# Performance work log

Hardware: AMD Instinct MI355X
Metric: run time of the kernel (lower is better)

## Reference

```python
import jax, jax.numpy as jnp
import numpy as np

IN_DIM = 256
CODE_LEN = 128
MEM_LEN = 65536
BETA = 1.0


def setup_inputs() -> dict:
    key = jax.random.key(0)
    k1, k2, k3, k4, k5, k6 = jax.random.split(key, 6)
    x = jax.random.normal(k1, (1, IN_DIM), dtype=jnp.float32)
    memory = jax.random.normal(k2, (MEM_LEN, CODE_LEN), dtype=jnp.float32)
    mem_data = jax.random.normal(k3, (MEM_LEN, IN_DIM), dtype=jnp.float32)
    mem_idx = jnp.arange(MEM_LEN, dtype=jnp.int64) if jax.config.jax_enable_x64 else jnp.arange(MEM_LEN, dtype=jnp.int32)
    W = jax.random.normal(k4, (CODE_LEN, IN_DIM), dtype=jnp.float32) / np.sqrt(IN_DIM)
    b = jax.random.normal(k5, (CODE_LEN,), dtype=jnp.float32) * 0.01
    count = jnp.array(0, dtype=jnp.int32)
    return {"x": x, "memory": memory, "mem_data": mem_data, "mem_idx": mem_idx,
            "W": W, "b": b, "count": count}


def reference(x, memory, mem_data, mem_idx, W, b, count):
    # mean/std normalization using memory bank statistics (torch .std uses ddof=1)
    mean = mem_data.mean(axis=0)                      # [in_dim]
    std = mem_data.std(axis=0, ddof=1)                # [in_dim]
    new = (x - mean) / std
    new = jnp.where(std == 0, 0.0, new)               # [1, in_dim]
    # linear encode
    enc = new @ W.T + b                               # [1, code_len]
    # L1 distance to every memory slot, take min
    dists = jnp.sum(jnp.abs(memory - enc), axis=1)    # [mem_len]
    loss = dists.min()
    # conditional scatter update of memory / mem_data / mem_idx
    do_update = loss <= BETA
    pos = jnp.argmin(mem_idx)
    new_memory = jnp.where(do_update,
                           memory.at[pos].set(enc[0]), memory)
    new_mem_data = jnp.where(do_update,
                             mem_data.at[pos].set(x[0]), mem_data)
    new_mem_idx = jnp.where(do_update,
                            mem_idx.at[pos].set(count.astype(mem_idx.dtype)), mem_idx)
    return loss, new_memory, new_mem_data, new_mem_idx
```

## Files before the change

kernel.cpp:

```cpp
#include <hip/hip_runtime.h>
#include <hip/hip_bf16.h>

#define IN_DIM   256
#define CODE_LEN 128
#define MEM_LEN  65536
#define BETA     1.0f

#define OUT_MEM_OFF   1
#define OUT_MD_OFF    (1 + MEM_LEN*CODE_LEN)
#define OUT_IDX_OFF   (OUT_MD_OFF + MEM_LEN*IN_DIM)

#define WS_COLSUM 0
#define WS_COLSQ  256
#define WS_ENC    512
#define WS_LOSS   640
#define WS_KEY    642

#define MD_ELEMS  (MEM_LEN*IN_DIM)
#define MD_TILES  ((MD_ELEMS-4)/4)
#define MEM_ELEMS (MEM_LEN*CODE_LEN)
#define MEM_STORE_TILES 2097151

__device__ __forceinline__ float4 load4u(const float* p) {
    float4 v; v.x = p[0]; v.y = p[1]; v.z = p[2]; v.w = p[3]; return v;
}

__global__ __launch_bounds__(512, 4) void k_stats_copy(
        const float* __restrict__ mem_data,
        const int*   __restrict__ mem_idx,
        float* __restrict__ out,
        float* __restrict__ ws) {
    if (blockIdx.x >= 512) {
        __shared__ unsigned long long red[512];
        const int t = threadIdx.x;
        const int tid = (blockIdx.x - 512) * 512 + t;
        unsigned long long local = ~0ull;
        #pragma unroll
        for (int rep = 0; rep < 2; ++rep) {
            int i = tid + rep * 32768;
            int v = mem_idx[i];
            out[OUT_IDX_OFF + i] = (float)v;
            unsigned long long key =
                (((unsigned long long)(unsigned int)(v ^ (int)0x80000000)) << 32)
                | (unsigned int)i;
            local = local < key ? local : key;
        }
        red[t] = local;
        __syncthreads();
        for (int s = 256; s > 0; s >>= 1) {
            if (t < s) { unsigned long long o = red[t + s]; if (o < red[t]) red[t] = o; }
            __syncthreads();
        }
        if (t == 0) atomicMin((unsigned long long*)(ws + WS_KEY), red[0]);
        return;
    }

    __shared__ float lsum[256], lsq[256];
    const int t = threadIdx.x;
    float* __restrict__ out_md = out + OUT_MD_OFF;
    const int t0 = blockIdx.x * 512 + t;
    float s0=0,s1=0,s2=0,s3=0,q0=0,q1=0,q2=0,q3=0;

    #pragma unroll 5
    for (int it = 0; it < 15; ++it) {
        const int k = t0 + it * 262144;
        const float* src = mem_data + 4*k + 3;
        float a0 = src[0], a1 = src[1], a2 = src[2], a3 = src[3];
        float4 v; v.x=a0; v.y=a1; v.z=a2; v.w=a3;
        *reinterpret_cast<float4*>(out_md + 4*k + 3) = v;
        s0 += a0; q0 += a0*a0;  s1 += a1; q1 += a1*a1;
        s2 += a2; q2 += a2*a2;  s3 += a3; q3 += a3*a3;
    }
    {
        const int k = t0 + 15 * 262144;
        if (k < MD_TILES) {
            const float* src = mem_data + 4*k + 3;
            float a0 = src[0], a1 = src[1], a2 = src[2], a3 = src[3];
            float4 v; v.x=a0; v.y=a1; v.z=a2; v.w=a3;
            *reinterpret_cast<float4*>(out_md + 4*k + 3) = v;
            s0 += a0; q0 += a0*a0;  s1 += a1; q1 += a1*a1;
            s2 += a2; q2 += a2*a2;  s3 += a3; q3 += a3*a3;
        }
    }

    if (t < 256) { lsum[t] = 0.f; lsq[t] = 0.f; }
    __syncthreads();
    const int c0 = (4*t0 + 3) & 255;
    atomicAdd(&lsum[c0],         s0);  atomicAdd(&lsq[c0],         q0);
    atomicAdd(&lsum[(c0+1)&255], s1);  atomicAdd(&lsq[(c0+1)&255], q1);
    atomicAdd(&lsum[(c0+2)&255], s2);  atomicAdd(&lsq[(c0+2)&255], q2);
    atomicAdd(&lsum[(c0+3)&255], s3);  atomicAdd(&lsq[(c0+3)&255], q3);
    __syncthreads();
    if (t < 256) {
        atomicAdd(&ws[WS_COLSUM + t], lsum[t]);
        atomicAdd(&ws[WS_COLSQ  + t], lsq[t]);
    }

    if (blockIdx.x == 0 && t == 0) {
        for (int e2 = 0; e2 < 3; ++e2) {
            float v = mem_data[e2];
            out_md[e2] = v;
            atomicAdd(&ws[WS_COLSUM + e2], v);
            atomicAdd(&ws[WS_COLSQ  + e2], v*v);
        }
        float v = mem_data[MD_ELEMS - 1];
        out_md[MD_ELEMS - 1] = v;
        atomicAdd(&ws[WS_COLSUM + 255], v);
        atomicAdd(&ws[WS_COLSQ  + 255], v*v);
    }
}

__global__ void k_enc(const float* __restrict__ x,
                      const float* __restrict__ W,
                      const float* __restrict__ b,
                      float* __restrict__ ws) {
    __shared__ float nrm[IN_DIM];
    const int t = threadIdx.x;
    float sum = ws[WS_COLSUM + t];
    float sq  = ws[WS_COLSQ + t];
    float mean = sum * (1.0f / MEM_LEN);
    float var  = (sq - sum * sum * (1.0f / MEM_LEN)) * (1.0f / (MEM_LEN - 1));
    var = fmaxf(var, 0.0f);
    float sd = sqrtf(var);
    nrm[t] = (sd == 0.0f) ? 0.0f : (x[t] - mean) / sd;
    __syncthreads();
    if (t < CODE_LEN) {
        float acc = b[t];
        const float* w = W + t * IN_DIM;
        #pragma unroll 8
        for (int d = 0; d < IN_DIM; ++d) acc += nrm[d] * w[d];
        ws[WS_ENC + t] = acc;
    }
}

__global__ __launch_bounds__(256, 4) void k_dist_copy(
        const float* __restrict__ memory,
        float* __restrict__ out,
        float* __restrict__ ws) {
    __shared__ float4 es[32];
    __shared__ float red[256];
    const int t = threadIdx.x;
    if (t < 32) es[t] = ((const float4*)(ws + WS_ENC))[t];
    __syncthreads();
    const int lane = t & 31;
    const int grp  = t >> 5;
    const float4 e = es[lane];
    float* __restrict__ out_al = out + 4;
    float localmin = 3.4e38f;
    #pragma unroll 2
    for (int sweep = 0; sweep < 8; ++sweep) {
        const int row = sweep * 8192 + blockIdx.x * 8 + grp;
        const int i = row * 32 + lane;
        float4 m = ((const float4*)memory)[i];
        if (i < MEM_STORE_TILES) {
            float4 s = load4u(memory + 4*i + 3);
            *reinterpret_cast<float4*>(out_al + 4*i) = s;
        }
        float d = fabsf(m.x-e.x) + fabsf(m.y-e.y) + fabsf(m.z-e.z) + fabsf(m.w-e.w);
        #pragma unroll
        for (int off = 16; off > 0; off >>= 1) d += __shfl_xor(d, off, 32);
        localmin = fminf(localmin, d);
    }
    red[t] = localmin;
    __syncthreads();
    for (int s2 = 128; s2 > 0; s2 >>= 1) {
        if (t < s2) red[t] = fminf(red[t], red[t + s2]);
        __syncthreads();
    }
    if (t == 0)
        atomicMin((unsigned int*)(ws + WS_LOSS), __float_as_uint(red[0]));
    if (blockIdx.x == 0 && t == 0) {
        float* om = out + OUT_MEM_OFF;
        om[0] = memory[0]; om[1] = memory[1]; om[2] = memory[2];
        om[MEM_ELEMS - 1] = memory[MEM_ELEMS - 1];
    }
}

__global__ void k_final(const float* __restrict__ x,
                        const int* __restrict__ count,
                        const float* __restrict__ ws,
                        float* __restrict__ d_out) {
    const int t = threadIdx.x;
    const float loss = __uint_as_float(((const unsigned int*)ws)[WS_LOSS]);
    if (t == 0) d_out[0] = loss;
    if (loss <= BETA) {
        unsigned long long key = *(const unsigned long long*)(ws + WS_KEY);
        unsigned int pos = (unsigned int)(key & 0xFFFFFFFFull);
        if (t < CODE_LEN)
            d_out[OUT_MEM_OFF + (size_t)pos * CODE_LEN + t] = ws[WS_ENC + t];
        d_out[OUT_MD_OFF + (size_t)pos * IN_DIM + t] = x[t];
        if (t == 0)
            d_out[OUT_IDX_OFF + pos] = (float)count[0];
    }
}

extern "C" void kernel_launch(void* const* d_in, const int* in_sizes, int n_in,
                              void* d_out, int out_size, void* d_ws, size_t ws_size,
                              hipStream_t stream) {
    const float* x        = (const float*)d_in[0];
    const float* memory   = (const float*)d_in[1];
    const float* mem_data = (const float*)d_in[2];
    const int*   mem_idx  = (const int*)d_in[3];
    const float* W        = (const float*)d_in[4];
    const float* b        = (const float*)d_in[5];
    const int*   count    = (const int*)d_in[6];
    float* out = (float*)d_out;
    float* ws  = (float*)d_ws;

    hipMemsetAsync(ws, 0, 2048, stream);
    hipMemsetAsync((char*)ws + 2560, 0xFF, 16, stream);

    k_stats_copy<<<576, 512, 0, stream>>>(mem_data, mem_idx, out, ws);
    k_enc<<<1, 256, 0, stream>>>(x, W, b, ws);
    k_dist_copy<<<1024, 256, 0, stream>>>(memory, out, ws);
    k_final<<<1, 256, 0, stream>>>(x, count, ws, out);
}
```

Before: 226.7 us.

## Batch loads with nontemporal stores and replace memsets with an init kernel

Both copy kernels now issue all their loads first and then their stores, so more memory requests are in flight per thread. Stores use nontemporal hints, which reduces cache pollution on the large output streams. The stats kernel is retuned to 1088 blocks of 256 threads, and the two hipMemsetAsync calls are replaced by one small init kernel to cut launch overhead. Batching the loads raises register pressure, which may reduce occupancy.

Result: no change. 226.0 us (-0.3%).

```diff
diff --git a/kernel.cpp b/kernel.cpp
--- a/kernel.cpp
+++ b/kernel.cpp
@@ -21,23 +21,36 @@
 #define MEM_ELEMS (MEM_LEN*CODE_LEN)
 #define MEM_STORE_TILES 2097151
 
-__device__ __forceinline__ float4 load4u(const float* p) {
-    float4 v; v.x = p[0]; v.y = p[1]; v.z = p[2]; v.w = p[3]; return v;
-}
-
-__global__ __launch_bounds__(512, 4) void k_stats_copy(
+typedef float vfloat4 __attribute__((ext_vector_type(4)));
+
+__device__ __forceinline__ vfloat4 load4u(const float* p) {
+    vfloat4 v; v.x = p[0]; v.y = p[1]; v.z = p[2]; v.w = p[3]; return v;
+}
+
+__global__ void k_init(float* __restrict__ ws) {
+    const int t = threadIdx.x;
+    #pragma unroll
+    for (int j = 0; j < 8; ++j) ws[t + j * 64] = 0.f;
+    if (t == 0) {
+        ((unsigned int*)ws)[WS_LOSS] = 0xFFFFFFFFu;
+        *((unsigned long long*)(ws + WS_KEY)) = ~0ull;
+    }
+}
+
+__global__ __launch_bounds__(256, 4) void k_stats_copy(
         const float* __restrict__ mem_data,
         const int*   __restrict__ mem_idx,
         float* __restrict__ out,
         float* __restrict__ ws) {
-    if (blockIdx.x >= 512) {
-        __shared__ unsigned long long red[512];
-        const int t = threadIdx.x;
-        const int tid = (blockIdx.x - 512) * 512 + t;
+    const int t = threadIdx.x;
+
+    if (blockIdx.x >= 1024) {
+        __shared__ unsigned long long red[256];
+        const int tid = (blockIdx.x - 1024) * 256 + t;
         unsigned long long local = ~0ull;
         #pragma unroll
-        for (int rep = 0; rep < 2; ++rep) {
-            int i = tid + rep * 32768;
+        for (int rep = 0; rep < 4; ++rep) {
+            int i = tid + rep * 16384;
             int v = mem_idx[i];
             out[OUT_IDX_OFF + i] = (float)v;
             unsigned long long key =
@@ -47,7 +60,7 @@
         }
         red[t] = local;
         __syncthreads();
-        for (int s = 256; s > 0; s >>= 1) {
+        for (int s = 128; s > 0; s >>= 1) {
             if (t < s) { unsigned long long o = red[t + s]; if (o < red[t]) red[t] = o; }
             __syncthreads();
         }
@@ -56,34 +69,34 @@
     }
 
     __shared__ float lsum[256], lsq[256];
-    const int t = threadIdx.x;
     float* __restrict__ out_md = out + OUT_MD_OFF;
-    const int t0 = blockIdx.x * 512 + t;
+    const int t0 = blockIdx.x * 256 + t;
     float s0=0,s1=0,s2=0,s3=0,q0=0,q1=0,q2=0,q3=0;
 
-    #pragma unroll 5
-    for (int it = 0; it < 15; ++it) {
-        const int k = t0 + it * 262144;
-        const float* src = mem_data + 4*k + 3;
-        float a0 = src[0], a1 = src[1], a2 = src[2], a3 = src[3];
-        float4 v; v.x=a0; v.y=a1; v.z=a2; v.w=a3;
-        *reinterpret_cast<float4*>(out_md + 4*k + 3) = v;
-        s0 += a0; q0 += a0*a0;  s1 += a1; q1 += a1*a1;
-        s2 += a2; q2 += a2*a2;  s3 += a3; q3 += a3*a3;
-    }
-    {
-        const int k = t0 + 15 * 262144;
-        if (k < MD_TILES) {
-            const float* src = mem_data + 4*k + 3;
-            float a0 = src[0], a1 = src[1], a2 = src[2], a3 = src[3];
-            float4 v; v.x=a0; v.y=a1; v.z=a2; v.w=a3;
-            *reinterpret_cast<float4*>(out_md + 4*k + 3) = v;
-            s0 += a0; q0 += a0*a0;  s1 += a1; q1 += a1*a1;
-            s2 += a2; q2 += a2*a2;  s3 += a3; q3 += a3*a3;
-        }
-    }
-
-    if (t < 256) { lsum[t] = 0.f; lsq[t] = 0.f; }
+    #pragma unroll
+    for (int g = 0; g < 2; ++g) {
+        vfloat4 v[8];
+        #pragma unroll
+        for (int j = 0; j < 8; ++j) {
+            const int k = t0 + (g * 8 + j) * 262144;
+            if (k < MD_TILES) v[j] = load4u(mem_data + 4*k + 3);
+            else              v[j] = (vfloat4){0.f, 0.f, 0.f, 0.f};
+        }
+        #pragma unroll
+        for (int j = 0; j < 8; ++j) {
+            const int k = t0 + (g * 8 + j) * 262144;
+            if (k < MD_TILES) {
+                __builtin_nontemporal_store(v[j],
+                    reinterpret_cast<vfloat4*>(out_md + 4*k + 3));
+                s0 += v[j].x; q0 += v[j].x * v[j].x;
+                s1 += v[j].y; q1 += v[j].y * v[j].y;
+                s2 += v[j].z; q2 += v[j].z * v[j].z;
+                s3 += v[j].w; q3 += v[j].w * v[j].w;
+            }
+        }
+    }
+
+    lsum[t] = 0.f; lsq[t] = 0.f;
     __syncthreads();
     const int c0 = (4*t0 + 3) & 255;
     atomicAdd(&lsum[c0],         s0);  atomicAdd(&lsq[c0],         q0);
@@ -91,17 +104,15 @@
     atomicAdd(&lsum[(c0+2)&255], s2);  atomicAdd(&lsq[(c0+2)&255], q2);
     atomicAdd(&lsum[(c0+3)&255], s3);  atomicAdd(&lsq[(c0+3)&255], q3);
     __syncthreads();
-    if (t < 256) {
-        atomicAdd(&ws[WS_COLSUM + t], lsum[t]);
-        atomicAdd(&ws[WS_COLSQ  + t], lsq[t]);
-    }
+    atomicAdd(&ws[WS_COLSUM + t], lsum[t]);
+    atomicAdd(&ws[WS_COLSQ  + t], lsq[t]);
 
     if (blockIdx.x == 0 && t == 0) {
-        for (int e2 = 0; e2 < 3; ++e2) {
-            float v = mem_data[e2];
-            out_md[e2] = v;
-            atomicAdd(&ws[WS_COLSUM + e2], v);
-            atomicAdd(&ws[WS_COLSQ  + e2], v*v);
+        for (int e = 0; e < 3; ++e) {
+            float v = mem_data[e];
+            out_md[e] = v;
+            atomicAdd(&ws[WS_COLSUM + e], v);
+            atomicAdd(&ws[WS_COLSQ  + e], v*v);
         }
         float v = mem_data[MD_ELEMS - 1];
         out_md[MD_ELEMS - 1] = v;
@@ -137,29 +148,41 @@
         const float* __restrict__ memory,
         float* __restrict__ out,
         float* __restrict__ ws) {
-    __shared__ float4 es[32];
+    __shared__ vfloat4 es[32];
     __shared__ float red[256];
     const int t = threadIdx.x;
-    if (t < 32) es[t] = ((const float4*)(ws + WS_ENC))[t];
+    if (t < 32) es[t] = ((const vfloat4*)(ws + WS_ENC))[t];
     __syncthreads();
     const int lane = t & 31;
     const int grp  = t >> 5;
-    const float4 e = es[lane];
+    const vfloat4 e = es[lane];
     float* __restrict__ out_al = out + 4;
     float localmin = 3.4e38f;
-    #pragma unroll 2
-    for (int sweep = 0; sweep < 8; ++sweep) {
-        const int row = sweep * 8192 + blockIdx.x * 8 + grp;
-        const int i = row * 32 + lane;
-        float4 m = ((const float4*)memory)[i];
-        if (i < MEM_STORE_TILES) {
-            float4 s = load4u(memory + 4*i + 3);
-            *reinterpret_cast<float4*>(out_al + 4*i) = s;
-        }
-        float d = fabsf(m.x-e.x) + fabsf(m.y-e.y) + fabsf(m.z-e.z) + fabsf(m.w-e.w);
-        #pragma unroll
-        for (int off = 16; off > 0; off >>= 1) d += __shfl_xor(d, off, 32);
-        localmin = fminf(localmin, d);
+    #pragma unroll
+    for (int half = 0; half < 2; ++half) {
+        vfloat4 m[4], s[4];
+        int idx[4];
+        #pragma unroll
+        for (int sw = 0; sw < 4; ++sw) {
+            const int row = (half * 4 + sw) * 8192 + blockIdx.x * 8 + grp;
+            const int i = row * 32 + lane;
+            idx[sw] = i;
+            m[sw] = ((const vfloat4*)memory)[i];
+            s[sw] = (i < MEM_STORE_TILES) ? load4u(memory + 4*i + 3)
+                                          : (vfloat4){0.f, 0.f, 0.f, 0.f};
+        }
+        #pragma unroll
+        for (int sw = 0; sw < 4; ++sw) {
+            const int i = idx[sw];
+            if (i < MEM_STORE_TILES)
+                __builtin_nontemporal_store(s[sw],
+                    reinterpret_cast<vfloat4*>(out_al + 4*i));
+            float d = fabsf(m[sw].x-e.x) + fabsf(m[sw].y-e.y)
+                    + fabsf(m[sw].z-e.z) + fabsf(m[sw].w-e.w);
+            #pragma unroll
+            for (int off = 16; off > 0; off >>= 1) d += __shfl_xor(d, off, 32);
+            localmin = fminf(localmin, d);
+        }
     }
     red[t] = localmin;
     __syncthreads();
@@ -207,10 +230,8 @@
     float* out = (float*)d_out;
     float* ws  = (float*)d_ws;
 
-    hipMemsetAsync(ws, 0, 2048, stream);
-    hipMemsetAsync((char*)ws + 2560, 0xFF, 16, stream);
-
-    k_stats_copy<<<576, 512, 0, stream>>>(mem_data, mem_idx, out, ws);
+    k_init<<<1, 64, 0, stream>>>(ws);
+    k_stats_copy<<<1088, 256, 0, stream>>>(mem_data, mem_idx, out, ws);
     k_enc<<<1, 256, 0, stream>>>(x, W, b, ws);
     k_dist_copy<<<1024, 256, 0, stream>>>(memory, out, ws);
     k_final<<<1, 256, 0, stream>>>(x, count, ws, out);
```
